# Optimization experiments

Measured on AMD Instinct MI355X. Metric: run time of the kernel, lower is better.

The kernel has to match this reference:

```python
import math
import jax, jax.numpy as jnp
import numpy as np

MODEL_DIM = 2048
NUM_EXPERTS = 64
NUM_TOKENS = 8192
CAPACITY_FACTOR = 1.0


def setup_inputs() -> dict:
    key = jax.random.key(0)
    kx, kw = jax.random.split(key)
    x = jax.random.normal(kx, (NUM_TOKENS, MODEL_DIM), dtype=jnp.float32)
    # Linear(model_dim, num_experts, bias=False): weight [E, D], y = x @ W.T
    wg = jax.random.normal(kw, (NUM_EXPERTS, MODEL_DIM), dtype=jnp.float32) * (1.0 / math.sqrt(MODEL_DIM))
    return {"x": x, "wg": wg}


def reference(x, wg):
    # ---- gate projection: logits [S, E] ----
    logits = jnp.einsum('sd,ed->se', x, wg)
    gates = jax.nn.softmax(logits, axis=1)
    S, E = gates.shape
    # training mode -> capacity = capacity_factor * ceil(S / E)  (static)
    capacity = int(CAPACITY_FACTOR * math.ceil(S / E))

    # ---- top-1 expert selection ----
    indices1_s = jnp.argmax(gates, axis=1)                      # [S]
    mask1 = jax.nn.one_hot(indices1_s, E, dtype=jnp.int32)      # [S, E]

    # gate value of the chosen expert per token
    gates1_s = jnp.sum(gates * mask1.astype(gates.dtype), axis=1)  # [S]

    # position of each token within its expert's queue (cumsum over tokens)
    locations1 = jnp.cumsum(mask1, axis=0) - 1                  # [S, E]

    # ---- load-balancing auxiliary loss ----
    me = jnp.mean(gates, axis=0)                                # [E]
    ce = jnp.mean(mask1.astype(gates.dtype), axis=0)            # [E]
    l_aux = jnp.mean(me * ce) * (E * E)

    # ---- capacity enforcement: drop tokens beyond expert capacity ----
    mask1 = mask1 * (locations1 < capacity).astype(mask1.dtype) # [S, E]
    locations1_s = jnp.sum(locations1 * mask1, axis=1)          # [S]

    # ---- combine / dispatch tensors ----
    gates1 = gates1_s[:, None] * mask1.astype(gates.dtype)      # [S, E]
    locations1_sc = jax.nn.one_hot(locations1_s, capacity, dtype=gates.dtype)  # [S, C]
    # torch.bmm(gates1[:, :, None], locations1_sc[:, None, :]) == outer product per token
    combine1_sec = jnp.einsum('se,sc->sec', gates1, locations1_sc)  # [S, E, C]
    dispatch_mask = combine1_sec > 0                            # bool [S, E, C]

    return l_aux, combine1_sec, dispatch_mask
```

## Files before the change

kernel.cpp:

```cpp
#include <hip/hip_runtime.h>
#include <math.h>

#define DIM     2048
#define NEXP    64
#define CAP     128
#define NTOK    8192
#define NTILE   256
#define KC      256
#define NCH     (DIM/KC)
#define XWSTR   260
#define PSTR    68

#define OUT_LAST   134217728ull

typedef float vfloat4 __attribute__((ext_vector_type(4)));

__global__ __launch_bounds__(256) void fill_out(float* __restrict__ out)
{
    vfloat4* o4 = reinterpret_cast<vfloat4*>(out);
    const vfloat4 z4 = {0.f, 0.f, 0.f, 0.f};
    size_t base = (size_t)blockIdx.x * 16384 + threadIdx.x;
    #pragma unroll 16
    for (int q = 0; q < 64; ++q)
        __builtin_nontemporal_store(z4, &o4[base + ((size_t)q << 8)]);
    if (blockIdx.x == 0 && threadIdx.x == 0)
        out[OUT_LAST] = 0.0f;
}

__global__ __launch_bounds__(256, 1) void gate_kernel(
    const float* __restrict__ x, const float* __restrict__ wg,
    int* __restrict__ expert_idx, float* __restrict__ gate_top,
    float* __restrict__ me_partial, int* __restrict__ counts)
{
    __shared__ __align__(16) float smem[(32 + NEXP) * XWSTR];
    __shared__ float me_w[4 * NEXP];
    __shared__ int   cnt_w[4 * NEXP];

    float* xs = smem;
    float* ws = smem + 32 * XWSTR;

    const int tid  = threadIdx.x;
    const int gb   = blockIdx.x;
    const int tok0 = gb * 32;
    const int s    = tid >> 5;
    const int i    = tid & 31;
    const int tg   = i & 3;
    const int eg   = i >> 2;
    const int kb   = s * 32;

    float acc[8][8] = {};

    for (int ch = 0; ch < NCH; ++ch) {
        const int k0 = ch * KC;
        #pragma unroll
        for (int q = 0; q < 8; ++q) {
            int id = tid + (q << 8);
            int r = id >> 6, c = id & 63;
            float4 v = *(const float4*)(x + (size_t)(tok0 + r) * DIM + k0 + 4 * c);
            *(float4*)(&xs[r * XWSTR + 4 * c]) = v;
        }
        #pragma unroll
        for (int q = 0; q < 16; ++q) {
            int id = tid + (q << 8);
            int r = id >> 6, c = id & 63;
            float4 v = *(const float4*)(wg + (size_t)r * DIM + k0 + 4 * c);
            *(float4*)(&ws[r * XWSTR + 4 * c]) = v;
        }
        __syncthreads();

        for (int q2 = 0; q2 < 8; ++q2) {
            const int kk = kb + 4 * q2;
            float4 xt[8], we[8];
            #pragma unroll
            for (int j = 0; j < 8; ++j)
                xt[j] = *(const float4*)(&xs[(tg + 4 * j) * XWSTR + kk]);
            #pragma unroll
            for (int m = 0; m < 8; ++m)
                we[m] = *(const float4*)(&ws[(eg + 8 * m) * XWSTR + kk]);
            #pragma unroll
            for (int j = 0; j < 8; ++j)
                #pragma unroll
                for (int m = 0; m < 8; ++m) {
                    acc[j][m] = fmaf(xt[j].x, we[m].x, acc[j][m]);
                    acc[j][m] = fmaf(xt[j].y, we[m].y, acc[j][m]);
                    acc[j][m] = fmaf(xt[j].z, we[m].z, acc[j][m]);
                    acc[j][m] = fmaf(xt[j].w, we[m].w, acc[j][m]);
                }
        }
        __syncthreads();
    }

    float* part = smem;
    float* lgt  = smem + 8 * 32 * PSTR;
    #pragma unroll
    for (int j = 0; j < 8; ++j)
        #pragma unroll
        for (int m = 0; m < 8; ++m)
            part[(s * 32 + tg + 4 * j) * PSTR + eg + 8 * m] = acc[j][m];
    __syncthreads();

    {
        int t  = tid >> 3;
        int e0 = (tid & 7) * 8;
        float4 a0 = {0,0,0,0}, a1 = {0,0,0,0};
        #pragma unroll
        for (int s2 = 0; s2 < 8; ++s2) {
            float4 p0 = *(const float4*)(&part[(s2 * 32 + t) * PSTR + e0]);
            float4 p1 = *(const float4*)(&part[(s2 * 32 + t) * PSTR + e0 + 4]);
            a0.x += p0.x; a0.y += p0.y; a0.z += p0.z; a0.w += p0.w;
            a1.x += p1.x; a1.y += p1.y; a1.z += p1.z; a1.w += p1.w;
        }
        __syncthreads();
        *(float4*)(&lgt[t * PSTR + e0])     = a0;
        *(float4*)(&lgt[t * PSTR + e0 + 4]) = a1;
    }
    __syncthreads();

    const int lane = tid & 63;
    const int wv   = tid >> 6;
    float me_acc  = 0.0f;
    int   cnt_acc = 0;
    for (int r8 = 0; r8 < 8; ++r8) {
        int row = wv * 8 + r8;
        float v = lgt[row * PSTR + lane];
        float m = v; int mi = lane;
        #pragma unroll
        for (int off = 32; off > 0; off >>= 1) {
            float om  = __shfl_xor(m, off);
            int   omi = __shfl_xor(mi, off);
            if (om > m || (om == m && omi < mi)) { m = om; mi = omi; }
        }
        float ex = __expf(v - m);
        float sm = ex;
        #pragma unroll
        for (int off = 32; off > 0; off >>= 1) sm += __shfl_xor(sm, off);
        me_acc += ex / sm;
        if (lane == mi) {
            expert_idx[tok0 + row] = mi;
            gate_top[tok0 + row]   = 1.0f / sm;
            ++cnt_acc;
        }
    }
    me_w[wv * NEXP + lane]  = me_acc;
    cnt_w[wv * NEXP + lane] = cnt_acc;
    __syncthreads();
    if (tid < NEXP) {
        me_partial[gb * NEXP + tid] = me_w[tid] + me_w[NEXP + tid]
                                    + me_w[2 * NEXP + tid] + me_w[3 * NEXP + tid];
        counts[gb * NEXP + tid]     = cnt_w[tid] + cnt_w[NEXP + tid]
                                    + cnt_w[2 * NEXP + tid] + cnt_w[3 * NEXP + tid];
    }
}

__global__ __launch_bounds__(1024) void prefix_laux(
    const float* __restrict__ me_partial, const int* __restrict__ counts,
    int* __restrict__ block_off, float* __restrict__ out)
{
    __shared__ int   cnt_l[16 * NEXP];
    __shared__ float me_l[16 * NEXP];
    __shared__ int   cnt_tot[NEXP];
    __shared__ float me_tot[NEXP];

    const int tid = threadIdx.x;
    const int e   = tid & 63;
    const int g   = tid >> 6;

    int cs = 0; float ms = 0.f;
    #pragma unroll
    for (int i = 0; i < 16; ++i) {
        int t = g * 16 + i;
        cs += counts[t * NEXP + e];
        ms += me_partial[t * NEXP + e];
    }
    cnt_l[g * NEXP + e] = cs;
    me_l[g * NEXP + e]  = ms;
    __syncthreads();

    if (g == 0) {
        int run = 0; float mt = 0.f;
        #pragma unroll
        for (int i = 0; i < 16; ++i) {
            int c = cnt_l[i * NEXP + e];
            cnt_l[i * NEXP + e] = run;
            run += c;
            mt  += me_l[i * NEXP + e];
        }
        cnt_tot[e] = run;
        me_tot[e]  = mt;
    }
    __syncthreads();

    int run = cnt_l[g * NEXP + e];
    #pragma unroll
    for (int i = 0; i < 16; ++i) {
        int t = g * 16 + i;
        block_off[t * NEXP + e] = run;
        run += counts[t * NEXP + e];
    }

    if (tid < NEXP) {
        float v = (me_tot[e] / (float)NTOK) * ((float)cnt_tot[e] / (float)NTOK);
        #pragma unroll
        for (int off = 32; off > 0; off >>= 1) v += __shfl_xor(v, off);
        if (e == 0) out[0] = v * (float)NEXP;
    }
}

__global__ __launch_bounds__(64) void scatter_k(
    const int* __restrict__ expert_idx, const float* __restrict__ gate_top,
    const int* __restrict__ block_off, float* __restrict__ out)
{
    __shared__ int es[32];
    int t = threadIdx.x, b = blockIdx.x;
    if (t < 32) es[t] = expert_idx[b * 32 + t];
    __syncthreads();
    if (t < 32) {
        int e = es[t];
        int rank = 0;
        for (int u = 0; u < t; ++u) rank += (es[u] == e) ? 1 : 0;
        int loc = block_off[b * NEXP + e] + rank;
        if (loc < CAP) {
            size_t sidx = (size_t)(b * 32 + t);
            size_t off  = sidx * (NEXP * CAP) + (size_t)e * CAP + loc;
            out[1 + off] = gate_top[b * 32 + t];
            out[1 + (size_t)NTOK * NEXP * CAP + off] = 1.0f;
        }
    }
}

extern "C" void kernel_launch(void* const* d_in, const int* in_sizes, int n_in,
                              void* d_out, int out_size, void* d_ws, size_t ws_size,
                              hipStream_t stream)
{
    const float* x  = (const float*)d_in[0];
    const float* wg = (const float*)d_in[1];
    float* out = (float*)d_out;

    char* ws = (char*)d_ws;
    int*   expert_idx = (int*)  (ws);
    float* gate_top   = (float*)(ws + 32768);
    float* me_partial = (float*)(ws + 65536);
    int*   counts     = (int*)  (ws + 131072);
    int*   block_off  = (int*)  (ws + 196608);

    fill_out<<<2048, 256, 0, stream>>>(out);
    gate_kernel<<<NTILE, 256, 0, stream>>>(x, wg, expert_idx, gate_top,
                                           me_partial, counts);
    prefix_laux<<<1, 1024, 0, stream>>>(me_partial, counts, block_off, out);
    scatter_k<<<NTILE, 64, 0, stream>>>(expert_idx, gate_top, block_off, out);
}
```

Baseline: 615.5 us.

## Fuse zero-fill and scatter into one dense emit pass; widen gate kernel to 512 threads

Removes the separate zero-fill kernel and the scatter kernel. The prefix kernel now computes a single one-hot column index per token, and a new emit kernel writes both 256MB output regions in one dense pass with the payload filled in. This avoids a second scattered write over a region that was just zeroed. The gate kernel moves to 512 threads with a split-K reduction through shared memory and computes per-tile ranks in-kernel. In exchange, the emit kernel does per-element compare logic and writes unaligned float4s offset by the leading l_aux scalar.

After: 617.4 us. No clear change (+0.3%).

```diff
diff --git a/kernel.cpp b/kernel.cpp
--- a/kernel.cpp
+++ b/kernel.cpp
@@ -10,31 +10,20 @@
 #define NCH     (DIM/KC)
 #define XWSTR   260
 #define PSTR    68
-
-#define OUT_LAST   134217728ull
+#define RF      67108864
 
 typedef float vfloat4 __attribute__((ext_vector_type(4)));
 
-__global__ __launch_bounds__(256) void fill_out(float* __restrict__ out)
-{
-    vfloat4* o4 = reinterpret_cast<vfloat4*>(out);
-    const vfloat4 z4 = {0.f, 0.f, 0.f, 0.f};
-    size_t base = (size_t)blockIdx.x * 16384 + threadIdx.x;
-    #pragma unroll 16
-    for (int q = 0; q < 64; ++q)
-        __builtin_nontemporal_store(z4, &o4[base + ((size_t)q << 8)]);
-    if (blockIdx.x == 0 && threadIdx.x == 0)
-        out[OUT_LAST] = 0.0f;
-}
-
-__global__ __launch_bounds__(256, 1) void gate_kernel(
+__global__ __launch_bounds__(512, 2) void gate_kernel(
     const float* __restrict__ x, const float* __restrict__ wg,
     int* __restrict__ expert_idx, float* __restrict__ gate_top,
+    int* __restrict__ rank,
     float* __restrict__ me_partial, int* __restrict__ counts)
 {
     __shared__ __align__(16) float smem[(32 + NEXP) * XWSTR];
-    __shared__ float me_w[4 * NEXP];
-    __shared__ int   cnt_w[4 * NEXP];
+    __shared__ float me_w[8 * NEXP];
+    __shared__ int   cnt_w[8 * NEXP];
+    __shared__ int   exp_s[32];
 
     float* xs = smem;
     float* ws = smem + 32 * XWSTR;
@@ -42,33 +31,34 @@
     const int tid  = threadIdx.x;
     const int gb   = blockIdx.x;
     const int tok0 = gb * 32;
-    const int s    = tid >> 5;
+    const int sl   = tid >> 5;
     const int i    = tid & 31;
     const int tg   = i & 3;
     const int eg   = i >> 2;
-    const int kb   = s * 32;
+    const int kb   = sl * 16;
 
     float acc[8][8] = {};
 
     for (int ch = 0; ch < NCH; ++ch) {
         const int k0 = ch * KC;
         #pragma unroll
-        for (int q = 0; q < 8; ++q) {
-            int id = tid + (q << 8);
+        for (int q = 0; q < 4; ++q) {
+            int id = tid + (q << 9);
             int r = id >> 6, c = id & 63;
             float4 v = *(const float4*)(x + (size_t)(tok0 + r) * DIM + k0 + 4 * c);
             *(float4*)(&xs[r * XWSTR + 4 * c]) = v;
         }
         #pragma unroll
-        for (int q = 0; q < 16; ++q) {
-            int id = tid + (q << 8);
+        for (int q = 0; q < 8; ++q) {
+            int id = tid + (q << 9);
             int r = id >> 6, c = id & 63;
             float4 v = *(const float4*)(wg + (size_t)r * DIM + k0 + 4 * c);
             *(float4*)(&ws[r * XWSTR + 4 * c]) = v;
         }
         __syncthreads();
 
-        for (int q2 = 0; q2 < 8; ++q2) {
+        #pragma unroll
+        for (int q2 = 0; q2 < 4; ++q2) {
             const int kk = kb + 4 * q2;
             float4 xt[8], we[8];
             #pragma unroll
@@ -92,27 +82,35 @@
 
     float* part = smem;
     float* lgt  = smem + 8 * 32 * PSTR;
-    #pragma unroll
-    for (int j = 0; j < 8; ++j)
-        #pragma unroll
-        for (int m = 0; m < 8; ++m)
-            part[(s * 32 + tg + 4 * j) * PSTR + eg + 8 * m] = acc[j][m];
+    if (sl >= 8) {
+        #pragma unroll
+        for (int j = 0; j < 8; ++j)
+            #pragma unroll
+            for (int m = 0; m < 8; ++m)
+                part[((sl - 8) * 32 + tg + 4 * j) * PSTR + eg + 8 * m] = acc[j][m];
+    }
+    __syncthreads();
+    if (sl < 8) {
+        #pragma unroll
+        for (int j = 0; j < 8; ++j)
+            #pragma unroll
+            for (int m = 0; m < 8; ++m) {
+                int idx = ((sl) * 32 + tg + 4 * j) * PSTR + eg + 8 * m;
+                part[idx] += acc[j][m];
+            }
+    }
     __syncthreads();
 
     {
-        int t  = tid >> 3;
-        int e0 = (tid & 7) * 8;
-        float4 a0 = {0,0,0,0}, a1 = {0,0,0,0};
+        int t  = tid >> 4;
+        int e0 = (tid & 15) << 2;
+        float4 a = {0, 0, 0, 0};
         #pragma unroll
         for (int s2 = 0; s2 < 8; ++s2) {
-            float4 p0 = *(const float4*)(&part[(s2 * 32 + t) * PSTR + e0]);
-            float4 p1 = *(const float4*)(&part[(s2 * 32 + t) * PSTR + e0 + 4]);
-            a0.x += p0.x; a0.y += p0.y; a0.z += p0.z; a0.w += p0.w;
-            a1.x += p1.x; a1.y += p1.y; a1.z += p1.z; a1.w += p1.w;
-        }
-        __syncthreads();
-        *(float4*)(&lgt[t * PSTR + e0])     = a0;
-        *(float4*)(&lgt[t * PSTR + e0 + 4]) = a1;
+            float4 p = *(const float4*)(&part[(s2 * 32 + t) * PSTR + e0]);
+            a.x += p.x; a.y += p.y; a.z += p.z; a.w += p.w;
+        }
+        *(float4*)(&lgt[t * PSTR + e0]) = a;
     }
     __syncthreads();
 
@@ -120,8 +118,9 @@
     const int wv   = tid >> 6;
     float me_acc  = 0.0f;
     int   cnt_acc = 0;
-    for (int r8 = 0; r8 < 8; ++r8) {
-        int row = wv * 8 + r8;
+    #pragma unroll
+    for (int r4 = 0; r4 < 4; ++r4) {
+        int row = wv * 4 + r4;
         float v = lgt[row * PSTR + lane];
         float m = v; int mi = lane;
         #pragma unroll
@@ -138,24 +137,35 @@
         if (lane == mi) {
             expert_idx[tok0 + row] = mi;
             gate_top[tok0 + row]   = 1.0f / sm;
+            exp_s[row] = mi;
             ++cnt_acc;
         }
     }
     me_w[wv * NEXP + lane]  = me_acc;
     cnt_w[wv * NEXP + lane] = cnt_acc;
     __syncthreads();
+
+    if (tid < 32) {
+        int e = exp_s[tid];
+        int rk = 0;
+        for (int u = 0; u < tid; ++u) rk += (exp_s[u] == e) ? 1 : 0;
+        rank[tok0 + tid] = rk;
+    }
     if (tid < NEXP) {
-        me_partial[gb * NEXP + tid] = me_w[tid] + me_w[NEXP + tid]
-                                    + me_w[2 * NEXP + tid] + me_w[3 * NEXP + tid];
-        counts[gb * NEXP + tid]     = cnt_w[tid] + cnt_w[NEXP + tid]
-                                    + cnt_w[2 * NEXP + tid] + cnt_w[3 * NEXP + tid];
+        float ms = 0.f; int cs = 0;
+        #pragma unroll
+        for (int w = 0; w < 8; ++w) { ms += me_w[w * NEXP + tid]; cs += cnt_w[w * NEXP + tid]; }
+        me_partial[gb * NEXP + tid] = ms;
+        counts[gb * NEXP + tid]     = cs;
     }
 }
 
 __global__ __launch_bounds__(1024) void prefix_laux(
     const float* __restrict__ me_partial, const int* __restrict__ counts,
-    int* __restrict__ block_off, float* __restrict__ out)
-{
+    const int* __restrict__ expert_idx, const int* __restrict__ rank,
+    int* __restrict__ hot, float* __restrict__ out)
+{
+    __shared__ int   bo_l[NTILE * NEXP];
     __shared__ int   cnt_l[16 * NEXP];
     __shared__ float me_l[16 * NEXP];
     __shared__ int   cnt_tot[NEXP];
@@ -194,9 +204,10 @@
     #pragma unroll
     for (int i = 0; i < 16; ++i) {
         int t = g * 16 + i;
-        block_off[t * NEXP + e] = run;
+        bo_l[t * NEXP + e] = run;
         run += counts[t * NEXP + e];
     }
+    __syncthreads();
 
     if (tid < NEXP) {
         float v = (me_tot[e] / (float)NTOK) * ((float)cnt_tot[e] / (float)NTOK);
@@ -204,28 +215,58 @@
         for (int off = 32; off > 0; off >>= 1) v += __shfl_xor(v, off);
         if (e == 0) out[0] = v * (float)NEXP;
     }
-}
-
-__global__ __launch_bounds__(64) void scatter_k(
-    const int* __restrict__ expert_idx, const float* __restrict__ gate_top,
-    const int* __restrict__ block_off, float* __restrict__ out)
-{
-    __shared__ int es[32];
-    int t = threadIdx.x, b = blockIdx.x;
-    if (t < 32) es[t] = expert_idx[b * 32 + t];
-    __syncthreads();
-    if (t < 32) {
-        int e = es[t];
-        int rank = 0;
-        for (int u = 0; u < t; ++u) rank += (es[u] == e) ? 1 : 0;
-        int loc = block_off[b * NEXP + e] + rank;
-        if (loc < CAP) {
-            size_t sidx = (size_t)(b * 32 + t);
-            size_t off  = sidx * (NEXP * CAP) + (size_t)e * CAP + loc;
-            out[1 + off] = gate_top[b * 32 + t];
-            out[1 + (size_t)NTOK * NEXP * CAP + off] = 1.0f;
-        }
-    }
+
+    #pragma unroll
+    for (int ii = 0; ii < 8; ++ii) {
+        int s  = tid + (ii << 10);
+        int ex = expert_idx[s];
+        int loc = bo_l[(s >> 5) * NEXP + ex] + rank[s];
+        hot[s] = (loc < CAP) ? (ex * CAP + loc) : -1;
+    }
+}
+
+__global__ __launch_bounds__(256) void emit_out(
+    const int* __restrict__ hot, const float* __restrict__ pay,
+    float* __restrict__ out)
+{
+    __shared__ int   hot_l[5];
+    __shared__ float pay_l[5];
+
+    const int tid = threadIdx.x;
+    const int b   = blockIdx.x;
+    const int reg = b >> 11;
+    const int zb  = b & 2047;
+    const int s0  = zb * 4;
+
+    if (tid < 5) {
+        int s = s0 + tid;
+        bool ok = (s < NTOK);
+        hot_l[tid] = ok ? hot[s] : -1;
+        pay_l[tid] = ok ? ((reg == 0) ? pay[s] : 1.0f) : 0.0f;
+    }
+    __syncthreads();
+
+    float* base = out + (size_t)reg * RF + 4;
+    #pragma unroll 8
+    for (int q = 0; q < 32; ++q) {
+        int i4 = zb * 8192 + tid + (q << 8);
+        if (i4 < 16777215) {
+            int r0 = 4 * i4 + 3;
+            vfloat4 v;
+            #pragma unroll
+            for (int k = 0; k < 4; ++k) {
+                int r  = r0 + k;
+                int sl = (r >> 13) - s0;
+                int w  = r & 8191;
+                v[k] = (w == hot_l[sl]) ? pay_l[sl] : 0.0f;
+            }
+            *(vfloat4*)(base + (size_t)4 * i4) = v;
+        }
+    }
+    if (zb == 0 && tid < 3)
+        out[(size_t)reg * RF + 1 + tid] = (tid == hot_l[0]) ? pay_l[0] : 0.0f;
+    if (zb == 2047 && tid == 0)
+        out[(size_t)reg * RF + RF] = (8191 == hot_l[3]) ? pay_l[3] : 0.0f;
 }
 
 extern "C" void kernel_launch(void* const* d_in, const int* in_sizes, int n_in,
@@ -239,13 +280,14 @@
     char* ws = (char*)d_ws;
     int*   expert_idx = (int*)  (ws);
     float* gate_top   = (float*)(ws + 32768);
-    float* me_partial = (float*)(ws + 65536);
-    int*   counts     = (int*)  (ws + 131072);
-    int*   block_off  = (int*)  (ws + 196608);
-
-    fill_out<<<2048, 256, 0, stream>>>(out);
-    gate_kernel<<<NTILE, 256, 0, stream>>>(x, wg, expert_idx, gate_top,
+    int*   rank       = (int*)  (ws + 65536);
+    float* me_partial = (float*)(ws + 98304);
+    int*   counts     = (int*)  (ws + 163840);
+    int*   hot        = (int*)  (ws + 229376);
+
+    gate_kernel<<<NTILE, 512, 0, stream>>>(x, wg, expert_idx, gate_top, rank,
                                            me_partial, counts);
-    prefix_laux<<<1, 1024, 0, stream>>>(me_partial, counts, block_off, out);
-    scatter_k<<<NTILE, 64, 0, stream>>>(expert_idx, gate_top, block_off, out);
-}
+    prefix_laux<<<1, 1024, 0, stream>>>(me_partial, counts, expert_idx, rank,
+                                        hot, out);
+    emit_out<<<4096, 256, 0, stream>>>(hot, gate_top, out);
+}
```
